# Performance work log

Hardware: AMD Instinct MI355X
Metric: run time of the kernel (lower is better)

## Reference

```python
import jax, jax.numpy as jnp
import numpy as np

T, B, H = 500, 256, 512

def setup_inputs() -> dict:
    key = jax.random.key(0)
    ks = jax.random.split(key, 7)
    s = 1.0 / np.sqrt(H)  # pytorch-style init scale
    return {
        "x": jax.random.normal(ks[0], (T, B, 1), dtype=jnp.float32),
        "w_ih": jax.random.uniform(ks[1], (4 * H, 1), minval=-s, maxval=s, dtype=jnp.float32),
        "w_hh": jax.random.uniform(ks[2], (4 * H, H), minval=-s, maxval=s, dtype=jnp.float32),
        "b_ih": jax.random.uniform(ks[3], (4 * H,), minval=-s, maxval=s, dtype=jnp.float32),
        "b_hh": jax.random.uniform(ks[4], (4 * H,), minval=-s, maxval=s, dtype=jnp.float32),
        "w_lin": jax.random.uniform(ks[5], (1, H), minval=-s, maxval=s, dtype=jnp.float32),
        "b_lin": jax.random.uniform(ks[6], (1,), minval=-s, maxval=s, dtype=jnp.float32),
    }

def _lstm_last_h(x, w_ih, w_hh, b_ih, b_hh):
    # x: (T, B, 1). Precompute input projection for all steps: (T, B, 4H)
    x_proj = jnp.einsum("tbi,gi->tbg", x, w_ih) + b_ih + b_hh
    Bsz = x.shape[1]
    Hsz = w_hh.shape[1]
    h0 = jnp.zeros((Bsz, Hsz), dtype=x.dtype)
    c0 = jnp.zeros((Bsz, Hsz), dtype=x.dtype)

    def step(carry, xp):
        h, c = carry
        gates = xp + h @ w_hh.T  # (B, 4H); pytorch gate order i, f, g, o
        i, f, g, o = jnp.split(gates, 4, axis=-1)
        i = jax.nn.sigmoid(i)
        f = jax.nn.sigmoid(f)
        g = jnp.tanh(g)
        o = jax.nn.sigmoid(o)
        c = f * c + i * g
        h = o * jnp.tanh(c)
        return (h, c), None

    (h_last, _), _ = jax.lax.scan(step, (h0, c0), x_proj)
    return h_last  # (B, H)

def reference(x, w_ih, w_hh, b_ih, b_hh, w_lin, b_lin):
    h_last = _lstm_last_h(x, w_ih, w_hh, b_ih, b_hh)
    return h_last @ w_lin.T + b_lin  # (B, 1)
```

## Files before the change

kernel.cpp:

```cpp
#include <hip/hip_runtime.h>
#include <hip/hip_fp16.h>

#define T_STEPS 500
#define HBUF_STRIDE 40960
#define F8_SCALE    32768.0f
#define F8_INV      3.0517578125e-05f
#define POLL_CAP    4096

typedef _Float16 half_t;
typedef __attribute__((ext_vector_type(8))) _Float16 half8;
typedef __attribute__((ext_vector_type(4))) float    f32x4;
typedef unsigned int       u32;
typedef unsigned long long u64;


__device__ __forceinline__ float sigmoid_fast(float v) {
    return 1.f / (1.f + __expf(-v));
}
__device__ __forceinline__ float tanh_fast(float v) {
    float a = fabsf(v);
    float e = __expf(-2.f * a);
    float t = (1.f - e) / (1.f + e);
    return copysignf(t, v);
}

__device__ __forceinline__ u32 load_u32_cc(const u32* p) {
    u32 v;
    asm volatile("global_load_dword %0, %1, off sc0 sc1\ns_waitcnt vmcnt(0)"
                 : "=v"(v) : "v"(p) : "memory");
    return v;
}
__device__ __forceinline__ f32x4 load_f32x4_cc_async(const void* p) {
    f32x4 v;
    asm volatile("global_load_dwordx4 %0, %1, off sc0 sc1" : "=v"(v) : "v"(p));
    return v;
}
__device__ __forceinline__ void store_u64_cc(void* p, u64 v) {
    asm volatile("global_store_dwordx2 %0, %1, off sc0 sc1" :: "v"(p), "v"(v) : "memory");
}
__device__ __forceinline__ void store_u32_cc(void* p, u32 v) {
    asm volatile("global_store_dword %0, %1, off sc0 sc1" :: "v"(p), "v"(v) : "memory");
}
__device__ __forceinline__ void wait_vm0() {
    asm volatile("s_waitcnt vmcnt(0)" ::: "memory");
}

__global__ __launch_bounds__(512, 2) void lstm_persist(
    const float* __restrict__ x,     const float* __restrict__ w_ih,
    const float* __restrict__ w_hh,  const float* __restrict__ b_ih,
    const float* __restrict__ b_hh,  const float* __restrict__ w_lin,
    const float* __restrict__ b_lin, float* __restrict__ out,
    u32* flags, char* hbase)
{
    __shared__ __align__(16) char stageBuf[40960];
    __shared__ float gate_s[4][16][68];
    __shared__ float wb_s[4][64][2];
    __shared__ float xall[T_STEPS * 16];

    half8* ldsAhi = (half8*)stageBuf;
    half8* ldsAlo = (half8*)(stageBuf + 16384);
    long*  ldsA8  = (long*)(stageBuf + 32768);

    const int tid = threadIdx.x;
    const int bid = blockIdx.x;
    const int g   = bid & 15;
    const int j   = bid >> 4;
    const int U0  = j * 64;
    const int m0  = g * 16;

    const int wave = tid >> 6, lane = tid & 63;
    const int kg   = lane >> 4, l15 = lane & 15;
    const int gw   = wave >> 1;
    const int usub = (wave & 1) * 32;

    half8 bw0[16], bw1[16];
    long  b80[16], b81[16];
    {
        const int col0 = gw * 512 + U0 + usub + l15;
        const int col1 = col0 + 16;
#pragma unroll
        for (int ks = 0; ks < 16; ++ks) {
            const float* p0 = w_hh + col0 * 512 + ks * 32 + kg * 8;
            const float* p1 = w_hh + col1 * 512 + ks * 32 + kg * 8;
            float v0[8], v1[8];
            *(float4*)(v0)     = *(const float4*)p0;
            *(float4*)(v0 + 4) = *(const float4*)(p0 + 4);
            *(float4*)(v1)     = *(const float4*)p1;
            *(float4*)(v1 + 4) = *(const float4*)(p1 + 4);
            half8 w0h, w1h; float r0[8], r1[8];
#pragma unroll
            for (int q = 0; q < 8; ++q) {
                half_t a = (half_t)v0[q]; w0h[q] = a; r0[q] = (v0[q] - (float)a) * F8_SCALE;
                half_t b = (half_t)v1[q]; w1h[q] = b; r1[q] = (v1[q] - (float)b) * F8_SCALE;
            }
            bw0[ks] = w0h; bw1[ks] = w1h;
            int lo = __builtin_amdgcn_cvt_pk_fp8_f32(r0[0], r0[1], 0, false);
            lo     = __builtin_amdgcn_cvt_pk_fp8_f32(r0[2], r0[3], lo, true);
            int hi = __builtin_amdgcn_cvt_pk_fp8_f32(r0[4], r0[5], 0, false);
            hi     = __builtin_amdgcn_cvt_pk_fp8_f32(r0[6], r0[7], hi, true);
            b80[ks] = (long)(u32)lo | ((long)hi << 32);
            lo = __builtin_amdgcn_cvt_pk_fp8_f32(r1[0], r1[1], 0, false);
            lo = __builtin_amdgcn_cvt_pk_fp8_f32(r1[2], r1[3], lo, true);
            hi = __builtin_amdgcn_cvt_pk_fp8_f32(r1[4], r1[5], 0, false);
            hi = __builtin_amdgcn_cvt_pk_fp8_f32(r1[6], r1[7], hi, true);
            b81[ks] = (long)(u32)lo | ((long)hi << 32);
        }
    }

    if (tid < 256) {
        int gg = tid >> 6, ul = tid & 63;
        int col = gg * 512 + U0 + ul;
        wb_s[gg][ul][0] = w_ih[col];
        wb_s[gg][ul][1] = b_ih[col] + b_hh[col];
    }
    for (int i = tid; i < T_STEPS * 16; i += 512)
        xall[i] = x[(i >> 4) * 256 + m0 + (i & 15)];

    u32* gflags = flags + g * 32;

    const int pm  = tid >> 4;
    const int pu4 = (tid & 15) * 4;
    const int kbg = j * 8 + (pu4 >> 3);
    const int off_hi = kbg * 256 + pm * 16 + (pu4 & 7) * 2;
    const int off_8  = kbg * 128 + pm * 8  + (pu4 & 7);
    float c4[4] = {0.f, 0.f, 0.f, 0.f};
    float h4[4] = {0.f, 0.f, 0.f, 0.f};

    {
        char* z = hbase + (g * 2 + 1) * HBUF_STRIDE;
#pragma unroll
        for (int r = 0; r < 10; ++r)
            store_u64_cc(z + (r * 512 + tid) * 8, 0ull);
    }
    wait_vm0();
    __syncthreads();
    if (tid == 0) store_u32_cc(&gflags[j], 1u);

    for (int t = 0; t < T_STEPS; ++t) {
        const int wb = t & 1, rb = wb ^ 1;

        if (tid < 8) {
            const u32 want = (u32)(t + 1);
            int it = 0;
            while (load_u32_cc(&gflags[tid]) < want && ++it < POLL_CAP)
                __builtin_amdgcn_s_sleep(2);
        }
        __syncthreads();

        {
            const char* p = hbase + (g * 2 + rb) * HBUF_STRIDE + tid * 16;
            f32x4 t0 = load_f32x4_cc_async(p);
            f32x4 t1 = load_f32x4_cc_async(p + 8192);
            f32x4 t2 = load_f32x4_cc_async(p + 16384);
            f32x4 t3 = load_f32x4_cc_async(p + 24576);
            f32x4 t4 = load_f32x4_cc_async(p + 32768);
            wait_vm0();
            f32x4* dst = (f32x4*)stageBuf;
            dst[tid] = t0; dst[512 + tid] = t1; dst[1024 + tid] = t2;
            dst[1536 + tid] = t3; dst[2048 + tid] = t4;
        }
        __syncthreads();

        f32x4 acc0 = {0.f, 0.f, 0.f, 0.f};
        f32x4 acc1 = {0.f, 0.f, 0.f, 0.f};
        f32x4 c80  = {0.f, 0.f, 0.f, 0.f};
        f32x4 c81  = {0.f, 0.f, 0.f, 0.f};
#pragma unroll
        for (int ks = 0; ks < 16; ++ks) {
            const int ai = (ks * 4 + kg) * 16 + l15;
            half8 ahi = ldsAhi[ai];
            half8 alo = ldsAlo[ai];
            long  a8  = ldsA8[ai];
            acc0 = __builtin_amdgcn_mfma_f32_16x16x32_f16(ahi, bw0[ks], acc0, 0, 0, 0);
            acc1 = __builtin_amdgcn_mfma_f32_16x16x32_f16(ahi, bw1[ks], acc1, 0, 0, 0);
            acc0 = __builtin_amdgcn_mfma_f32_16x16x32_f16(alo, bw0[ks], acc0, 0, 0, 0);
            acc1 = __builtin_amdgcn_mfma_f32_16x16x32_f16(alo, bw1[ks], acc1, 0, 0, 0);
            c80  = __builtin_amdgcn_mfma_f32_16x16x32_fp8_fp8(a8, b80[ks], c80, 0, 0, 0);
            c81  = __builtin_amdgcn_mfma_f32_16x16x32_fp8_fp8(a8, b81[ks], c81, 0, 0, 0);
        }
#pragma unroll
        for (int e = 0; e < 4; ++e) {
            gate_s[gw][kg * 4 + e][usub + l15]      = acc0[e] + c80[e] * F8_INV;
            gate_s[gw][kg * 4 + e][usub + 16 + l15] = acc1[e] + c81[e] * F8_INV;
        }
        __syncthreads();

        if (tid < 256) {
            float xv = xall[t * 16 + pm];
            float sg[4][4];
#pragma unroll
            for (int gg2 = 0; gg2 < 4; ++gg2) {
                float4 a  = *(float4*)&gate_s[gg2][pm][pu4];
                float4 wA = *(float4*)&wb_s[gg2][pu4][0];
                float4 wB = *(float4*)&wb_s[gg2][pu4 + 2][0];
                sg[gg2][0] = a.x + xv * wA.x + wA.y;
                sg[gg2][1] = a.y + xv * wA.z + wA.w;
                sg[gg2][2] = a.z + xv * wB.x + wB.y;
                sg[gg2][3] = a.w + xv * wB.z + wB.w;
            }
#pragma unroll
            for (int q = 0; q < 4; ++q) {
                float ii = sigmoid_fast(sg[0][q]);
                float ff = sigmoid_fast(sg[1][q]);
                float gv = tanh_fast(sg[2][q]);
                float oo = sigmoid_fast(sg[3][q]);
                c4[q] = ff * c4[q] + ii * gv;
                h4[q] = oo * tanh_fast(c4[q]);
            }
            union { half_t h[4]; u64 u; } hiU, loU;
#pragma unroll
            for (int q = 0; q < 4; ++q) {
                half_t hh = (half_t)h4[q];
                hiU.h[q] = hh;
                loU.h[q] = (half_t)(h4[q] - (float)hh);
            }
            int f8 = __builtin_amdgcn_cvt_pk_fp8_f32(h4[0], h4[1], 0, false);
            f8     = __builtin_amdgcn_cvt_pk_fp8_f32(h4[2], h4[3], f8, true);

            char* wrb = hbase + (g * 2 + wb) * HBUF_STRIDE;
            store_u64_cc(wrb + off_hi, hiU.u);
            store_u64_cc(wrb + 16384 + off_hi, loU.u);
            store_u32_cc(wrb + 32768 + off_8, (u32)f8);
        }
        wait_vm0();
        __syncthreads();
        if (tid == 0) store_u32_cc(&gflags[j], (u32)(t + 2));
    }

    if (tid < 256) {
        float part = h4[0] * w_lin[U0 + pu4]     + h4[1] * w_lin[U0 + pu4 + 1]
                   + h4[2] * w_lin[U0 + pu4 + 2] + h4[3] * w_lin[U0 + pu4 + 3];
        part += __shfl_xor(part, 1, 64);
        part += __shfl_xor(part, 2, 64);
        part += __shfl_xor(part, 4, 64);
        part += __shfl_xor(part, 8, 64);
        if ((tid & 15) == 0) {
            float v = part;
            if (j == 0) v += b_lin[0];
            atomicAdd(out + m0 + pm, v);
        }
    }
}

extern "C" void kernel_launch(void* const* d_in, const int* in_sizes, int n_in,
                              void* d_out, int out_size, void* d_ws, size_t ws_size,
                              hipStream_t stream) {
    const float* x     = (const float*)d_in[0];
    const float* w_ih  = (const float*)d_in[1];
    const float* w_hh  = (const float*)d_in[2];
    const float* b_ih  = (const float*)d_in[3];
    const float* b_hh  = (const float*)d_in[4];
    const float* w_lin = (const float*)d_in[5];
    const float* b_lin = (const float*)d_in[6];
    float* out = (float*)d_out;

    u32*  flags = (u32*)d_ws;
    char* hbase = (char*)d_ws + 4096;

    hipMemsetAsync(d_out, 0, out_size * sizeof(float), stream);
    hipMemsetAsync(d_ws, 0, 4096, stream);

    hipLaunchKernelGGL(lstm_persist, dim3(128), dim3(512), 0, stream,
                       x, w_ih, w_hh, b_ih, b_hh, w_lin, b_lin, out, flags, hbase);
}
```

Before: 2.263 ms.

## Drop low-half fp16 split of h and poll flags per wave

Removes the fp16 residual (lo) part of the hidden-state split, so the recurrent GEMM uses only fp16 hi plus the fp8 correction term. This halves the f16 MFMA count and shrinks the per-step global exchange buffer and LDS staging from 40 KB to 24 KB. Flag polling now happens in every wave, each wave checking its own producer block's flag, and each wave loads only that producer's slice. This drops the pre-load barrier and the s_sleep backoff. The cost is lower accuracy in h@W_hh, since the fp16 rounding residual is no longer represented, and busier spinning on the flags.

Result: faster. 1.862 ms (-17.7%).

```diff
diff --git a/kernel.cpp b/kernel.cpp
--- a/kernel.cpp
+++ b/kernel.cpp
@@ -2,7 +2,7 @@
 #include <hip/hip_fp16.h>
 
 #define T_STEPS 500
-#define HBUF_STRIDE 40960
+#define HBUF_STRIDE 24576
 #define F8_SCALE    32768.0f
 #define F8_INV      3.0517578125e-05f
 #define POLL_CAP    4096
@@ -52,14 +52,13 @@
     const float* __restrict__ b_lin, float* __restrict__ out,
     u32* flags, char* hbase)
 {
-    __shared__ __align__(16) char stageBuf[40960];
+    __shared__ __align__(16) char stageBuf[24576];
     __shared__ float gate_s[4][16][68];
     __shared__ float wb_s[4][64][2];
     __shared__ float xall[T_STEPS * 16];
 
     half8* ldsAhi = (half8*)stageBuf;
-    half8* ldsAlo = (half8*)(stageBuf + 16384);
-    long*  ldsA8  = (long*)(stageBuf + 32768);
+    long*  ldsA8  = (long*)(stageBuf + 16384);
 
     const int tid = threadIdx.x;
     const int bid = blockIdx.x;
@@ -129,7 +128,7 @@
     {
         char* z = hbase + (g * 2 + 1) * HBUF_STRIDE;
 #pragma unroll
-        for (int r = 0; r < 10; ++r)
+        for (int r = 0; r < 6; ++r)
             store_u64_cc(z + (r * 512 + tid) * 8, 0ull);
     }
     wait_vm0();
@@ -138,26 +137,21 @@
 
     for (int t = 0; t < T_STEPS; ++t) {
         const int wb = t & 1, rb = wb ^ 1;
-
-        if (tid < 8) {
+        const char* src = hbase + (g * 2 + rb) * HBUF_STRIDE;
+
+        {
             const u32 want = (u32)(t + 1);
             int it = 0;
-            while (load_u32_cc(&gflags[tid]) < want && ++it < POLL_CAP)
-                __builtin_amdgcn_s_sleep(2);
-        }
-        __syncthreads();
-
-        {
-            const char* p = hbase + (g * 2 + rb) * HBUF_STRIDE + tid * 16;
-            f32x4 t0 = load_f32x4_cc_async(p);
-            f32x4 t1 = load_f32x4_cc_async(p + 8192);
-            f32x4 t2 = load_f32x4_cc_async(p + 16384);
-            f32x4 t3 = load_f32x4_cc_async(p + 24576);
-            f32x4 t4 = load_f32x4_cc_async(p + 32768);
+            while (load_u32_cc(&gflags[wave]) < want && ++it < POLL_CAP) {}
+            const int hoff = wave * 2048 + lane * 16;
+            const int foff = 16384 + wave * 1024 + lane * 16;
+            f32x4 t0 = load_f32x4_cc_async(src + hoff);
+            f32x4 t1 = load_f32x4_cc_async(src + hoff + 1024);
+            f32x4 t2 = load_f32x4_cc_async(src + foff);
             wait_vm0();
-            f32x4* dst = (f32x4*)stageBuf;
-            dst[tid] = t0; dst[512 + tid] = t1; dst[1024 + tid] = t2;
-            dst[1536 + tid] = t3; dst[2048 + tid] = t4;
+            *(f32x4*)(stageBuf + hoff)        = t0;
+            *(f32x4*)(stageBuf + hoff + 1024) = t1;
+            *(f32x4*)(stageBuf + foff)        = t2;
         }
         __syncthreads();
 
@@ -169,12 +163,9 @@
         for (int ks = 0; ks < 16; ++ks) {
             const int ai = (ks * 4 + kg) * 16 + l15;
             half8 ahi = ldsAhi[ai];
-            half8 alo = ldsAlo[ai];
             long  a8  = ldsA8[ai];
             acc0 = __builtin_amdgcn_mfma_f32_16x16x32_f16(ahi, bw0[ks], acc0, 0, 0, 0);
             acc1 = __builtin_amdgcn_mfma_f32_16x16x32_f16(ahi, bw1[ks], acc1, 0, 0, 0);
-            acc0 = __builtin_amdgcn_mfma_f32_16x16x32_f16(alo, bw0[ks], acc0, 0, 0, 0);
-            acc1 = __builtin_amdgcn_mfma_f32_16x16x32_f16(alo, bw1[ks], acc1, 0, 0, 0);
             c80  = __builtin_amdgcn_mfma_f32_16x16x32_fp8_fp8(a8, b80[ks], c80, 0, 0, 0);
             c81  = __builtin_amdgcn_mfma_f32_16x16x32_fp8_fp8(a8, b81[ks], c81, 0, 0, 0);
         }
@@ -207,20 +198,15 @@
                 c4[q] = ff * c4[q] + ii * gv;
                 h4[q] = oo * tanh_fast(c4[q]);
             }
-            union { half_t h[4]; u64 u; } hiU, loU;
-#pragma unroll
-            for (int q = 0; q < 4; ++q) {
-                half_t hh = (half_t)h4[q];
-                hiU.h[q] = hh;
-                loU.h[q] = (half_t)(h4[q] - (float)hh);
-            }
+            union { half_t h[4]; u64 u; } hiU;
+#pragma unroll
+            for (int q = 0; q < 4; ++q) hiU.h[q] = (half_t)h4[q];
             int f8 = __builtin_amdgcn_cvt_pk_fp8_f32(h4[0], h4[1], 0, false);
             f8     = __builtin_amdgcn_cvt_pk_fp8_f32(h4[2], h4[3], f8, true);
 
             char* wrb = hbase + (g * 2 + wb) * HBUF_STRIDE;
             store_u64_cc(wrb + off_hi, hiU.u);
-            store_u64_cc(wrb + 16384 + off_hi, loU.u);
-            store_u32_cc(wrb + 32768 + off_8, (u32)f8);
+            store_u32_cc(wrb + 16384 + off_8, (u32)f8);
         }
         wait_vm0();
         __syncthreads();
```
